# Optimization experiments

Measured on AMD Instinct MI355X. Metric: run time of the kernel, lower is better.

Reference implementation:

```python
import jax, jax.numpy as jnp
import numpy as np

B, S, D = 2, 2048, 1024
H, HD = 16, 64

def setup_inputs() -> dict:
    key = jax.random.key(0)
    k1, k2, k3 = jax.random.split(key, 3)
    x = jax.random.normal(k1, (B, S, D), dtype=jnp.float32)
    w_qkv = jax.random.normal(k2, (3 * D, D), dtype=jnp.float32) * (D ** -0.5)
    w_out = jax.random.normal(k3, (D, D), dtype=jnp.float32) * (D ** -0.5)
    return {"x": x, "w_qkv": w_qkv, "w_out": w_out}

def reference(x, w_qkv, w_out):
    scale = HD ** -0.5
    # qkv projection: torch Linear applies x @ W.T
    qkv = jnp.einsum('bsd,ed->bse', x, w_qkv)            # [B,S,3D]
    qkv = qkv.reshape(B, S, 3, H, HD)
    q, k, v = qkv[:, :, 0], qkv[:, :, 1], qkv[:, :, 2]   # [B,S,H,HD]
    # scores: explicit matmul-softmax-matmul (unfused, as in source)
    scores = jnp.einsum('bqhd,bkhd->bhqk', q, k) * scale  # [B,H,S,S]
    attn = jax.nn.softmax(scores, axis=-1)
    out = jnp.einsum('bhqk,bkhd->bqhd', attn, v)          # [B,S,H,HD]
    out = out.reshape(B, S, D)
    return jnp.einsum('bsd,ed->bse', out, w_out)
```

## Files before the change

### kernel.cpp

```cpp
#include <hip/hip_runtime.h>
#include <hip/hip_bf16.h>
#include <math.h>

#define B_ 2
#define S_ 2048
#define D_ 1024
#define H_ 16
#define HD_ 64

typedef short bf16x8 __attribute__((ext_vector_type(8)));
typedef short bf16x4 __attribute__((ext_vector_type(4)));
typedef float f32x4 __attribute__((ext_vector_type(4)));

#define MFMA32(a, b, c) __builtin_amdgcn_mfma_f32_16x16x32_bf16(a, b, c, 0, 0, 0)
#define MFMA16(a, b, c) __builtin_amdgcn_mfma_f32_16x16x16bf16_1k(a, b, c, 0, 0, 0)

static __device__ __forceinline__ unsigned short f2bf(float f) {
    union { float f; unsigned u; } v = {f};
    return (unsigned short)((v.u + 0x7fffu + ((v.u >> 16) & 1u)) >> 16);
}

static __device__ __forceinline__ unsigned pk2bf(float a, float b) {
    __hip_bfloat162 h = __float22bfloat162_rn(make_float2(a, b));
    unsigned r;
    __builtin_memcpy(&r, &h, 4);
    return r;
}

static __device__ __forceinline__ void gl2lds16(const void* g, void* l) {
    __builtin_amdgcn_global_load_lds((const __attribute__((address_space(1))) unsigned int*)g,
                                     (__attribute__((address_space(3))) unsigned int*)l,
                                     16, 0, 0);
}

static __device__ __forceinline__ bf16x8 scaleQ(bf16x8 v, float s) {
    union { bf16x8 v; unsigned u[4]; } a, r;
    a.v = v;
    #pragma unroll
    for (int i = 0; i < 4; ++i) {
        float lo = __uint_as_float(a.u[i] << 16);
        float hi = __uint_as_float(a.u[i] & 0xffff0000u);
        r.u[i] = pk2bf(lo * s, hi * s);
    }
    return r.v;
}

__global__ __launch_bounds__(256) void cvt_all(const float* __restrict__ x,
                                               const float* __restrict__ wq,
                                               const float* __restrict__ wo,
                                               unsigned short* __restrict__ xb,
                                               unsigned short* __restrict__ wqb,
                                               unsigned short* __restrict__ wob) {
    const int N0 = 1048576, N1 = 786432, N2 = 262144;
    int stride = gridDim.x * blockDim.x;
    for (int i = blockIdx.x * blockDim.x + threadIdx.x; i < N0 + N1 + N2; i += stride) {
        const float4* src; ushort4* dst; int j;
        if (i < N0)            { src = (const float4*)x;  dst = (ushort4*)xb;  j = i; }
        else if (i < N0 + N1)  { src = (const float4*)wq; dst = (ushort4*)wqb; j = i - N0; }
        else                   { src = (const float4*)wo; dst = (ushort4*)wob; j = i - N0 - N1; }
        float4 v = src[j];
        ushort4 o;
        o.x = f2bf(v.x); o.y = f2bf(v.y); o.z = f2bf(v.z); o.w = f2bf(v.w);
        dst[j] = o;
    }
}

template <int BN>
__global__ __launch_bounds__(256) void gemm_nt_b(const unsigned short* __restrict__ A,
                                                 const unsigned short* __restrict__ Bm,
                                                 void* __restrict__ Cout,
                                                 unsigned short* __restrict__ vtout,
                                                 int M, int N, int K, int c_bf16) {
    constexpr int BM = 128, BK = 32;
    constexpr int MI = (BN == 128) ? 4 : 2;
    constexpr int NI = 4;
    constexpr int SEGS = (BM + BN) / 16;
    __shared__ unsigned short As[BM * BK];
    __shared__ unsigned short Bs[BN * BK];

    const int tid = threadIdx.x;
    const int wave = tid >> 6, lane = tid & 63;
    const int m16 = lane & 15, quad = lane >> 4;
    const int wrow = (BN == 128) ? (wave >> 1) * 64 : wave * 32;
    const int wcol = (BN == 128) ? (wave & 1) * 64 : 0;
    const int row0 = blockIdx.y * BM, col0 = blockIdx.x * BN;

    const int lrow = lane >> 2;
    const int lk = (lane & 3) * 8;

    f32x4 acc[MI][NI] = {};

    for (int k0 = 0; k0 < K; k0 += BK) {
        __syncthreads();
        for (int s = wave; s < SEGS; s += 4) {
            if (s < BM / 16) {
                gl2lds16(&A[(size_t)(row0 + s * 16 + lrow) * K + k0 + lk],
                         &As[s * 16 * BK]);
            } else {
                int t = s - BM / 16;
                gl2lds16(&Bm[(size_t)(col0 + t * 16 + lrow) * K + k0 + lk],
                         &Bs[t * 16 * BK]);
            }
        }
        __asm__ volatile("s_waitcnt vmcnt(0)" ::: "memory");
        __syncthreads();

        bf16x8 af[MI], bfr[NI];
        #pragma unroll
        for (int mi = 0; mi < MI; ++mi)
            af[mi] = *(const bf16x8*)&As[(wrow + mi * 16 + m16) * BK + quad * 8];
        #pragma unroll
        for (int ni = 0; ni < NI; ++ni)
            bfr[ni] = *(const bf16x8*)&Bs[(wcol + ni * 16 + m16) * BK + quad * 8];
        #pragma unroll
        for (int mi = 0; mi < MI; ++mi)
            #pragma unroll
            for (int ni = 0; ni < NI; ++ni)
                acc[mi][ni] = MFMA32(af[mi], bfr[ni], acc[mi][ni]);
    }

    if (vtout != nullptr && col0 >= 2 * D_) {
        #pragma unroll
        for (int mi = 0; mi < MI; ++mi) {
            int srow = row0 + wrow + mi * 16 + quad * 4;
            int bb = srow >> 11;
            int s = srow & (S_ - 1);
            #pragma unroll
            for (int ni = 0; ni < NI; ++ni) {
                int hd = col0 + wcol + ni * 16 + m16 - 2 * D_;
                ushort4 v4;
                v4.x = f2bf(acc[mi][ni][0]);
                v4.y = f2bf(acc[mi][ni][1]);
                v4.z = f2bf(acc[mi][ni][2]);
                v4.w = f2bf(acc[mi][ni][3]);
                *(ushort4*)&vtout[((size_t)(bb * 16 + (hd >> 6)) * 64 + (hd & 63)) * S_ + s] = v4;
            }
        }
        return;
    }

    #pragma unroll
    for (int mi = 0; mi < MI; ++mi) {
        #pragma unroll
        for (int r = 0; r < 4; ++r) {
            size_t grow = row0 + wrow + mi * 16 + quad * 4 + r;
            #pragma unroll
            for (int ni = 0; ni < NI; ++ni) {
                size_t gcol = col0 + wcol + ni * 16 + m16;
                if (c_bf16)
                    ((unsigned short*)Cout)[grow * N + gcol] = f2bf(acc[mi][ni][r]);
                else
                    ((float*)Cout)[grow * N + gcol] = acc[mi][ni][r];
            }
        }
    }
}

__global__ __launch_bounds__(512, 4) void attn_mfma(const unsigned short* __restrict__ qkv,
                                                    const unsigned short* __restrict__ vt,
                                                    unsigned short* __restrict__ out) {
    __shared__ unsigned short L[2][16384];

    const int id = blockIdx.x;
    const int bh = ((id >> 3) & 3) * 8 + (id & 7);
    const int b = bh >> 4, h = bh & 15;
    const int q0 = (id >> 5) * 128;

    const int tid = threadIdx.x;
    const int wave = tid >> 6, lane = tid & 63;
    const int grp = wave >> 2;
    const int qw = wave & 3;
    const int m16 = lane & 15, quad = lane >> 4;

    const float QS = 0.125f * 1.44269504089f;

    bf16x8 qf0[2], qf1[2];
    #pragma unroll
    for (int g = 0; g < 2; ++g) {
        const unsigned short* qrow =
            qkv + ((size_t)b * S_ + q0 + qw * 32 + g * 16 + m16) * (3 * D_) + h * HD_;
        qf0[g] = scaleQ(*(const bf16x8*)(qrow + quad * 8), QS);
        qf1[g] = scaleQ(*(const bf16x8*)(qrow + 32 + quad * 8), QS);
    }

    f32x4 o[2][4] = {};
    f32x4 ol[2] = {};
    const bf16x4 onesf = {(short)0x3F80, (short)0x3F80, (short)0x3F80, (short)0x3F80};

    const unsigned short* kbase = qkv + (size_t)b * S_ * 3 * D_ + D_ + h * HD_;
    const unsigned short* vtbase = vt + (size_t)bh * 64 * S_;

    const int lr8 = lane >> 3;
    const int lsrc = (lane & 7) ^ lr8;

    const int kaddr0 = m16 * 64 + ((quad ^ (m16 & 7)) * 8);
    const int kaddr1 = kaddr0 ^ 32;
    int va[4];
    #pragma unroll
    for (int nt = 0; nt < 4; ++nt) {
        int kc = nt * 2 + (quad >> 1);
        va[nt] = m16 * 64 + ((kc ^ (m16 & 7)) * 8) + (quad & 1) * 4;
    }

    auto issueDMA = [&](int pair, int buf) {
        const int mat = wave >> 1;
        const int tt = pair * 2 + (mat >> 1);
        unsigned short* dstb = &L[buf][mat * 4096];
        if ((mat & 1) == 0) {
            const unsigned short* kt = kbase + (size_t)tt * 64 * (3 * D_);
            #pragma unroll
            for (int i = 0; i < 4; ++i) {
                int gi = (wave & 1) * 4 + i;
                gl2lds16(kt + (size_t)(gi * 8 + lr8) * (3 * D_) + lsrc * 8,
                         dstb + gi * 512);
            }
        } else {
            const unsigned short* vtt = vtbase + tt * 64;
            #pragma unroll
            for (int i = 0; i < 4; ++i) {
                int gi = (wave & 1) * 4 + i;
                gl2lds16(vtt + (size_t)(gi * 8 + lr8) * S_ + lsrc * 8,
                         dstb + gi * 512);
            }
        }
    };

    issueDMA(0, 0);
    __asm__ volatile("s_waitcnt vmcnt(0)" ::: "memory");
    __syncthreads();
    issueDMA(1, 1);

    for (int s = 0; s < 16; ++s) {
        const int buf = s & 1;
        const unsigned short* Kp = &L[buf][grp * 8192];
        const unsigned short* Vp = Kp + 4096;

        bf16x4 pf[2][4];
        #pragma unroll
        for (int nt = 0; nt < 4; ++nt) {
            bf16x8 kf0 = *(const bf16x8*)&Kp[kaddr0 + nt * 1024];
            bf16x8 kf1 = *(const bf16x8*)&Kp[kaddr1 + nt * 1024];
            #pragma unroll
            for (int g = 0; g < 2; ++g) {
                f32x4 z = {0.f, 0.f, 0.f, 0.f};
                z = MFMA32(kf0, qf0[g], z);
                z = MFMA32(kf1, qf1[g], z);
                float p0 = __builtin_amdgcn_exp2f(z[0]);
                float p1 = __builtin_amdgcn_exp2f(z[1]);
                float p2 = __builtin_amdgcn_exp2f(z[2]);
                float p3 = __builtin_amdgcn_exp2f(z[3]);
                union { unsigned u[2]; bf16x4 v; } pk;
                pk.u[0] = pk2bf(p0, p1);
                pk.u[1] = pk2bf(p2, p3);
                pf[g][nt] = pk.v;
                ol[g] = MFMA16(pf[g][nt], onesf, ol[g]);
            }
        }

        #pragma unroll
        for (int nt = 0; nt < 4; ++nt)
            #pragma unroll
            for (int dt = 0; dt < 4; ++dt) {
                bf16x4 vf = *(const bf16x4*)&Vp[va[nt] + dt * 1024];
                o[0][dt] = MFMA16(pf[0][nt], vf, o[0][dt]);
                o[1][dt] = MFMA16(pf[1][nt], vf, o[1][dt]);
            }

        __asm__ volatile("s_waitcnt vmcnt(0)" ::: "memory");
        __syncthreads();
        if (s + 2 < 16) issueDMA(s + 2, buf);
    }

    float* M = (float*)&L[0][0];
    const int mb = (qw * 64 + lane) * 44;
    if (grp == 1) {
        #pragma unroll
        for (int g = 0; g < 2; ++g) {
            #pragma unroll
            for (int dt = 0; dt < 4; ++dt)
                *(f32x4*)&M[mb + (g * 4 + dt) * 4] = o[g][dt];
            *(f32x4*)&M[mb + 32 + g * 4] = ol[g];
        }
    }
    __syncthreads();
    if (grp == 0) {
        #pragma unroll
        for (int g = 0; g < 2; ++g) {
            #pragma unroll
            for (int dt = 0; dt < 4; ++dt)
                o[g][dt] += *(const f32x4*)&M[mb + (g * 4 + dt) * 4];
            ol[g] += *(const f32x4*)&M[mb + 32 + g * 4];
        }
        #pragma unroll
        for (int g = 0; g < 2; ++g)
            #pragma unroll
            for (int r = 0; r < 4; ++r) {
                float inv = 1.f / ol[g][r];
                size_t row = (size_t)b * S_ + q0 + qw * 32 + g * 16 + quad * 4 + r;
                unsigned short* op = out + row * D_ + h * HD_;
                #pragma unroll
                for (int dt = 0; dt < 4; ++dt)
                    op[dt * 16 + m16] = f2bf(o[g][dt][r] * inv);
            }
    }
}

extern "C" void kernel_launch(void* const* d_in, const int* in_sizes, int n_in,
                              void* d_out, int out_size, void* d_ws, size_t ws_size,
                              hipStream_t stream) {
    const float* x     = (const float*)d_in[0];
    const float* w_qkv = (const float*)d_in[1];
    const float* w_out = (const float*)d_in[2];
    float* out = (float*)d_out;

    const size_t n_x = (size_t)B_ * S_ * D_;
    const size_t n_wqkv = (size_t)3 * D_ * D_;
    const size_t n_wout = (size_t)D_ * D_;

    unsigned short* xb    = (unsigned short*)d_ws;
    unsigned short* wqkvb = xb + n_x;
    unsigned short* woutb = wqkvb + n_wqkv;
    unsigned short* qkvb  = woutb + n_wout;
    unsigned short* attnb = qkvb + (size_t)B_ * S_ * 3 * D_;
    unsigned short* vtb   = attnb + n_x;

    dim3 blk(256);

    cvt_all<<<2048, blk, 0, stream>>>(x, w_qkv, w_out, xb, wqkvb, woutb);

    gemm_nt_b<128><<<dim3(3 * D_ / 128, B_ * S_ / 128), blk, 0, stream>>>(
        xb, wqkvb, qkvb, vtb, B_ * S_, 3 * D_, D_, 1);

    attn_mfma<<<512, dim3(512), 0, stream>>>(qkvb, vtb, attnb);

    gemm_nt_b<64><<<dim3(D_ / 64, B_ * S_ / 128), blk, 0, stream>>>(
        attnb, woutb, out, nullptr, B_ * S_, D_, D_, 0);
}
```

Before: 196.0 us.

## Double-buffer GEMM LDS tiles and swizzle block order for L2 locality

The projection GEMM now keeps two LDS buffers and issues the global-to-LDS load for tile k+2 while computing on tile k, replacing the load-wait-compute loop with a pipelined one. Block indices are also remapped with a stride-8 interleave so that concurrently running blocks share A/B rows in cache. This doubles LDS usage per block, which may lower occupancy, and the remap assumes the block count divides by 8.

```diff
diff --git a/kernel.cpp b/kernel.cpp
--- a/kernel.cpp
+++ b/kernel.cpp
@@ -75,48 +75,63 @@
     constexpr int MI = (BN == 128) ? 4 : 2;
     constexpr int NI = 4;
     constexpr int SEGS = (BM + BN) / 16;
-    __shared__ unsigned short As[BM * BK];
-    __shared__ unsigned short Bs[BN * BK];
+    __shared__ unsigned short As[2][BM * BK];
+    __shared__ unsigned short Bs[2][BN * BK];
 
     const int tid = threadIdx.x;
     const int wave = tid >> 6, lane = tid & 63;
     const int m16 = lane & 15, quad = lane >> 4;
     const int wrow = (BN == 128) ? (wave >> 1) * 64 : wave * 32;
     const int wcol = (BN == 128) ? (wave & 1) * 64 : 0;
-    const int row0 = blockIdx.y * BM, col0 = blockIdx.x * BN;
+
+    const int nbx = gridDim.x;
+    const int nblk = nbx * gridDim.y;
+    const int lid = blockIdx.y * nbx + blockIdx.x;
+    const int id2 = (lid & 7) * (nblk >> 3) + (lid >> 3);
+    const int row0 = (id2 / nbx) * BM, col0 = (id2 % nbx) * BN;
 
     const int lrow = lane >> 2;
     const int lk = (lane & 3) * 8;
 
     f32x4 acc[MI][NI] = {};
 
-    for (int k0 = 0; k0 < K; k0 += BK) {
-        __syncthreads();
+    auto stage = [&](int kk, int buf) {
         for (int s = wave; s < SEGS; s += 4) {
             if (s < BM / 16) {
-                gl2lds16(&A[(size_t)(row0 + s * 16 + lrow) * K + k0 + lk],
-                         &As[s * 16 * BK]);
+                gl2lds16(&A[(size_t)(row0 + s * 16 + lrow) * K + kk * BK + lk],
+                         &As[buf][s * 16 * BK]);
             } else {
                 int t = s - BM / 16;
-                gl2lds16(&Bm[(size_t)(col0 + t * 16 + lrow) * K + k0 + lk],
-                         &Bs[t * 16 * BK]);
-            }
-        }
+                gl2lds16(&Bm[(size_t)(col0 + t * 16 + lrow) * K + kk * BK + lk],
+                         &Bs[buf][t * 16 * BK]);
+            }
+        }
+    };
+
+    const int nk = K / BK;
+    stage(0, 0);
+    __asm__ volatile("s_waitcnt vmcnt(0)" ::: "memory");
+    __syncthreads();
+    stage(1, 1);
+
+    for (int kk = 0; kk < nk; ++kk) {
+        const int buf = kk & 1;
+        bf16x8 af[MI], bfr[NI];
+        #pragma unroll
+        for (int mi = 0; mi < MI; ++mi)
+            af[mi] = *(const bf16x8*)&As[buf][(wrow + mi * 16 + m16) * BK + quad * 8];
+        #pragma unroll
+        for (int ni = 0; ni < NI; ++ni)
+            bfr[ni] = *(const bf16x8*)&Bs[buf][(wcol + ni * 16 + m16) * BK + quad * 8];
+        #pragma unroll
+        for (int mi = 0; mi < MI; ++mi)
+            #pragma unroll
+            for (int ni = 0; ni < NI; ++ni)
+                acc[mi][ni] = MFMA32(af[mi], bfr[ni], acc[mi][ni]);
+
         __asm__ volatile("s_waitcnt vmcnt(0)" ::: "memory");
         __syncthreads();
-
-        bf16x8 af[MI], bfr[NI];
-        #pragma unroll
-        for (int mi = 0; mi < MI; ++mi)
-            af[mi] = *(const bf16x8*)&As[(wrow + mi * 16 + m16) * BK + quad * 8];
-        #pragma unroll
-        for (int ni = 0; ni < NI; ++ni)
-            bfr[ni] = *(const bf16x8*)&Bs[(wcol + ni * 16 + m16) * BK + quad * 8];
-        #pragma unroll
-        for (int mi = 0; mi < MI; ++mi)
-            #pragma unroll
-            for (int ni = 0; ni < NI; ++ni)
-                acc[mi][ni] = MFMA32(af[mi], bfr[ni], acc[mi][ni]);
+        if (kk + 2 < nk) stage(kk + 2, buf);
     }
 
     if (vtout != nullptr && col0 >= 2 * D_) {
```

Measured after the change: 200.4 us. 1.02x slower.

## Double GEMM K-tile to 64 with XOR-swizzled LDS layout; raise wave priority in PV

Applied to the files above, without the earlier changes.

The projection GEMM now stages a 64-wide K slice per iteration instead of 32, which halves the number of barrier and wait rounds. The LDS tiles use an XOR swizzle on 16-byte chunks so the wider rows do not cause bank conflicts on fragment reads. The attention kernel raises wave scheduling priority around the PV MFMA block and passes a constant zero accumulator to the first score MFMA. The trade-off is more LDS per block and more registers for the doubled fragment set, which may lower occupancy.

```diff
diff --git a/kernel.cpp b/kernel.cpp
--- a/kernel.cpp
+++ b/kernel.cpp
@@ -71,10 +71,11 @@
                                                  void* __restrict__ Cout,
                                                  unsigned short* __restrict__ vtout,
                                                  int M, int N, int K, int c_bf16) {
-    constexpr int BM = 128, BK = 32;
+    constexpr int BM = 128, BK = 64;
     constexpr int MI = (BN == 128) ? 4 : 2;
     constexpr int NI = 4;
-    constexpr int SEGS = (BM + BN) / 16;
+    constexpr int ASEG = BM / 8;
+    constexpr int SEGS = (BM + BN) / 8;
     __shared__ unsigned short As[BM * BK];
     __shared__ unsigned short Bs[BN * BK];
 
@@ -85,38 +86,49 @@
     const int wcol = (BN == 128) ? (wave & 1) * 64 : 0;
     const int row0 = blockIdx.y * BM, col0 = blockIdx.x * BN;
 
-    const int lrow = lane >> 2;
-    const int lk = (lane & 3) * 8;
+    const int lr8 = lane >> 3;
+    const int lsrc = (lane & 7) ^ lr8;
+
+    const int ka = (quad ^ (m16 & 7)) * 8;
 
     f32x4 acc[MI][NI] = {};
 
-    for (int k0 = 0; k0 < K; k0 += BK) {
+    const int nk = K / BK;
+    for (int kk = 0; kk < nk; ++kk) {
         __syncthreads();
         for (int s = wave; s < SEGS; s += 4) {
-            if (s < BM / 16) {
-                gl2lds16(&A[(size_t)(row0 + s * 16 + lrow) * K + k0 + lk],
-                         &As[s * 16 * BK]);
+            if (s < ASEG) {
+                gl2lds16(&A[(size_t)(row0 + s * 8 + lr8) * K + kk * BK + lsrc * 8],
+                         &As[s * 8 * BK]);
             } else {
-                int t = s - BM / 16;
-                gl2lds16(&Bm[(size_t)(col0 + t * 16 + lrow) * K + k0 + lk],
-                         &Bs[t * 16 * BK]);
+                int t = s - ASEG;
+                gl2lds16(&Bm[(size_t)(col0 + t * 8 + lr8) * K + kk * BK + lsrc * 8],
+                         &Bs[t * 8 * BK]);
             }
         }
         __asm__ volatile("s_waitcnt vmcnt(0)" ::: "memory");
         __syncthreads();
 
-        bf16x8 af[MI], bfr[NI];
+        bf16x8 af0[MI], af1[MI], bf0[NI], bf1[NI];
+        #pragma unroll
+        for (int mi = 0; mi < MI; ++mi) {
+            int a = (wrow + mi * 16 + m16) * BK + ka;
+            af0[mi] = *(const bf16x8*)&As[a];
+            af1[mi] = *(const bf16x8*)&As[a ^ 32];
+        }
+        #pragma unroll
+        for (int ni = 0; ni < NI; ++ni) {
+            int a = (wcol + ni * 16 + m16) * BK + ka;
+            bf0[ni] = *(const bf16x8*)&Bs[a];
+            bf1[ni] = *(const bf16x8*)&Bs[a ^ 32];
+        }
         #pragma unroll
         for (int mi = 0; mi < MI; ++mi)
-            af[mi] = *(const bf16x8*)&As[(wrow + mi * 16 + m16) * BK + quad * 8];
-        #pragma unroll
-        for (int ni = 0; ni < NI; ++ni)
-            bfr[ni] = *(const bf16x8*)&Bs[(wcol + ni * 16 + m16) * BK + quad * 8];
-        #pragma unroll
-        for (int mi = 0; mi < MI; ++mi)
-            #pragma unroll
-            for (int ni = 0; ni < NI; ++ni)
-                acc[mi][ni] = MFMA32(af[mi], bfr[ni], acc[mi][ni]);
+            #pragma unroll
+            for (int ni = 0; ni < NI; ++ni) {
+                acc[mi][ni] = MFMA32(af0[mi], bf0[ni], acc[mi][ni]);
+                acc[mi][ni] = MFMA32(af1[mi], bf1[ni], acc[mi][ni]);
+            }
     }
 
     if (vtout != nullptr && col0 >= 2 * D_) {
@@ -185,6 +197,7 @@
 
     f32x4 o[2][4] = {};
     f32x4 ol[2] = {};
+    const f32x4 zf = {};
     const bf16x4 onesf = {(short)0x3F80, (short)0x3F80, (short)0x3F80, (short)0x3F80};
 
     const unsigned short* kbase = qkv + (size_t)b * S_ * 3 * D_ + D_ + h * HD_;
@@ -242,8 +255,7 @@
             bf16x8 kf1 = *(const bf16x8*)&Kp[kaddr1 + nt * 1024];
             #pragma unroll
             for (int g = 0; g < 2; ++g) {
-                f32x4 z = {0.f, 0.f, 0.f, 0.f};
-                z = MFMA32(kf0, qf0[g], z);
+                f32x4 z = MFMA32(kf0, qf0[g], zf);
                 z = MFMA32(kf1, qf1[g], z);
                 float p0 = __builtin_amdgcn_exp2f(z[0]);
                 float p1 = __builtin_amdgcn_exp2f(z[1]);
@@ -257,6 +269,7 @@
             }
         }
 
+        __builtin_amdgcn_s_setprio(1);
         #pragma unroll
         for (int nt = 0; nt < 4; ++nt)
             #pragma unroll
@@ -265,6 +278,7 @@
                 o[0][dt] = MFMA16(pf[0][nt], vf, o[0][dt]);
                 o[1][dt] = MFMA16(pf[1][nt], vf, o[1][dt]);
             }
+        __builtin_amdgcn_s_setprio(0);
 
         __asm__ volatile("s_waitcnt vmcnt(0)" ::: "memory");
         __syncthreads();
```

After: 180.6 us. -7.8%, faster.
